# Kernel optimization log

Measured on AMD Instinct MI355X. Metric: run time of the kernel, lower is better.

The kernel has to match this reference:

```python
import jax, jax.numpy as jnp
import numpy as np

BETA = 0.3        # SmoothL1Loss beta
LAMBDA_PHY = 0.15 # physics loss weight


def smooth_l1(d, beta):
    ad = jnp.abs(d)
    return jnp.where(ad < beta, 0.5 * d * d / beta, ad - 0.5 * beta)


def setup_inputs() -> dict:
    key = jax.random.key(0)
    k1, k2, k3, k4 = jax.random.split(key, 4)
    B, Z = 16384, 2048
    preds = jax.random.normal(k1, (B, Z, 1), dtype=jnp.float32)
    targets = jax.random.normal(k2, (B, Z), dtype=jnp.float32)
    current_temps = jax.random.normal(k3, (B, Z), dtype=jnp.float32)
    adjacency = jax.random.randint(k4, (Z, Z), 0, 2).astype(jnp.int32)
    return {"preds": preds, "targets": targets,
            "current_temps": current_temps, "adjacency": adjacency}


def reference(preds, targets, current_temps, adjacency):
    p = preds[:, :, 0]                               # [B, Z]
    num_zones = p.shape[1]
    pred_loss = smooth_l1(p - targets, BETA).mean()
    pred_change = p - current_temps                  # [B, Z]

    # Vectorized neighbor mean: replaces the per-zone Python loop with one
    # dense masked-adjacency contraction.
    mask = (adjacency > 0).astype(p.dtype)           # [Z, Z]
    deg = mask.sum(axis=1)                           # [Z]
    has_nb = deg > 0
    safe_deg = jnp.where(has_nb, deg, 1.0)
    avg_neighbor = jnp.einsum('zn,bn->bz', mask, current_temps) / safe_deg  # [B, Z]

    temp_diff = current_temps - avg_neighbor         # [B, Z]
    violation = jax.nn.softplus(temp_diff * pred_change)
    per_zone = violation.mean(axis=0)                # mean over batch, [Z]
    physics_loss = jnp.where(has_nb, per_zone, 0.0).sum() / num_zones

    total_loss = pred_loss + LAMBDA_PHY * physics_loss
    return (total_loss, physics_loss)
```

## Files before the change

kernel.cpp:

```cpp
#include <hip/hip_runtime.h>
#include <hip/hip_bf16.h>
#include <cmath>

#define BETA 0.3f
#define LAMBDA_PHY 0.15f

#define BM 128
#define BN 128
#define BK 64
#define NT 256

typedef __bf16 bf16x8 __attribute__((ext_vector_type(8)));
typedef float f32x4 __attribute__((ext_vector_type(4)));

#define AS1 __attribute__((address_space(1)))
#define AS3 __attribute__((address_space(3)))

#define FENCE() asm volatile("" ::: "memory")
#define BARRIER() do { FENCE(); __builtin_amdgcn_s_barrier(); FENCE(); } while (0)
#define WAITV8() asm volatile("s_waitcnt vmcnt(8)" ::: "memory")
#define WAITV0() asm volatile("s_waitcnt vmcnt(0)" ::: "memory")

__device__ __forceinline__ unsigned short f2bf_rn(float f) {
    unsigned int u = __builtin_bit_cast(unsigned int, f);
    return (unsigned short)((u + 0x7FFFu + ((u >> 16) & 1u)) >> 16);
}

__device__ __forceinline__ float bf2f(unsigned short u) {
    return __builtin_bit_cast(float, (unsigned int)u << 16);
}

__device__ __forceinline__ float softplus_f(float x) {
    return fmaxf(x, 0.0f) + __logf(1.0f + __expf(-fabsf(x)));
}

__device__ __forceinline__ float smooth_l1_f(float d) {
    float ad = fabsf(d);
    return (ad < BETA) ? (0.5f / BETA) * d * d : (ad - 0.5f * BETA);
}

__global__ void k_prep(const int* __restrict__ adj, unsigned short* __restrict__ maskbf,
                       float* __restrict__ invdeg, float* __restrict__ hasnb, int Z) {
    int z = blockIdx.x;
    int t = threadIdx.x;
    const int* row = adj + (size_t)z * Z;
    unsigned short* mrow = maskbf + (size_t)z * Z;
    int cnt = 0;
    for (int n = t; n < Z; n += blockDim.x) {
        int a = (row[n] > 0);
        mrow[n] = a ? (unsigned short)0x3F80 : (unsigned short)0;
        cnt += a;
    }
    for (int o = 32; o; o >>= 1) cnt += __shfl_down(cnt, o);
    __shared__ int rs[4];
    int lane = t & 63, wave = t >> 6;
    if (lane == 0) rs[wave] = cnt;
    __syncthreads();
    if (t == 0) {
        int deg = rs[0] + rs[1] + rs[2] + rs[3];
        invdeg[z] = (deg > 0) ? 1.0f / (float)deg : 1.0f;
        hasnb[z]  = (deg > 0) ? 1.0f : 0.0f;
    }
}

__global__ void k_conv(const float* __restrict__ src, uint4* __restrict__ dst, long n8) {
    long i = (long)blockIdx.x * blockDim.x + threadIdx.x;
    long stride = (long)gridDim.x * blockDim.x;
    for (; i < n8; i += stride) {
        const float4* s = (const float4*)(src + i * 8);
        float4 a = s[0], b = s[1];
        uint4 o;
        o.x = (unsigned)f2bf_rn(a.x) | ((unsigned)f2bf_rn(a.y) << 16);
        o.y = (unsigned)f2bf_rn(a.z) | ((unsigned)f2bf_rn(a.w) << 16);
        o.z = (unsigned)f2bf_rn(b.x) | ((unsigned)f2bf_rn(b.y) << 16);
        o.w = (unsigned)f2bf_rn(b.z) | ((unsigned)f2bf_rn(b.w) << 16);
        dst[i] = o;
    }
}

__global__ __launch_bounds__(NT, 2) void k_gemm(
    const unsigned short* __restrict__ Abf,
    const unsigned short* __restrict__ Bbf,
    const float* __restrict__ preds,
    const float* __restrict__ targets,
    const float* __restrict__ invdeg,
    const float* __restrict__ hasnb,
    float* __restrict__ partials,
    int M, int N, int K)
{
    __shared__ unsigned short AsF[2 * BM * 64];
    __shared__ unsigned short BsF[2 * BN * 64];

    const int nwg = gridDim.x;
    const int ob = blockIdx.x;
    const int bid = (nwg % 8 == 0) ? ((ob % 8) * (nwg / 8) + ob / 8) : ob;
    const int ntiles = N / BN;
    const int mt = bid / ntiles;
    const int nt = bid % ntiles;
    const int row0 = mt * BM;
    const int col0 = nt * BN;
    const int t = threadIdx.x;
    const int lane = t & 63;
    const int wave = t >> 6;
    const int wm = wave >> 1;
    const int wn = wave & 1;
    const int fr = lane & 15;
    const int fq = lane >> 4;
    const int fr7 = fr & 7;

    const int tr = t >> 3;
    const int tc = t & 7;
    const int cs = tc ^ (tr & 7);

    const int colk0 = (fq ^ fr7) * 8;
    const int colk1 = ((4 + fq) ^ fr7) * 8;
    const int ofsA0 = (wm * 64 + fr) * 64 + colk0;
    const int ofsA1 = (wm * 64 + fr) * 64 + colk1;
    const int ofsB0 = (wn * 64 + fr) * 64 + colk0;
    const int ofsB1 = (wn * 64 + fr) * 64 + colk1;

    f32x4 acc[4][4];
#pragma unroll
    for (int m = 0; m < 4; ++m)
#pragma unroll
        for (int n = 0; n < 4; ++n)
            acc[m][n] = (f32x4){0.f, 0.f, 0.f, 0.f};

    const unsigned short* aSrc = Abf + (size_t)(row0 + tr) * K + cs * 8;
    const unsigned short* bSrc = Bbf + (size_t)(col0 + tr) * K + cs * 8;
    unsigned short* aDstC = &AsF[t * 8];
    unsigned short* bDstC = &BsF[t * 8];

#define STAGE(BUF) do {                                                                      \
    _Pragma("unroll")                                                                        \
    for (int r_ = 0; r_ < 4; ++r_)                                                           \
        __builtin_amdgcn_global_load_lds((const AS1 void*)(aSrc + (size_t)(r_ * 32) * K),    \
                                         (AS3 void*)(aDstC + (BUF) * 8192 + r_ * 2048), 16, 0, 0); \
    _Pragma("unroll")                                                                        \
    for (int r_ = 0; r_ < 4; ++r_)                                                           \
        __builtin_amdgcn_global_load_lds((const AS1 void*)(bSrc + (size_t)(r_ * 32) * K),    \
                                         (AS3 void*)(bDstC + (BUF) * 8192 + r_ * 2048), 16, 0, 0); \
    aSrc += BK; bSrc += BK;                                                                  \
} while (0)

#define MFMA_KK(BUF, OFSA, OFSB) do {                                                        \
    bf16x8 af_[4], bv_[4];                                                                   \
    _Pragma("unroll")                                                                        \
    for (int mi_ = 0; mi_ < 4; ++mi_)                                                        \
        af_[mi_] = *(const bf16x8*)(AsF + (BUF) * 8192 + (OFSA) + mi_ * 1024);               \
    _Pragma("unroll")                                                                        \
    for (int ni_ = 0; ni_ < 4; ++ni_)                                                        \
        bv_[ni_] = *(const bf16x8*)(BsF + (BUF) * 8192 + (OFSB) + ni_ * 1024);               \
    __builtin_amdgcn_s_setprio(1);                                                           \
    _Pragma("unroll")                                                                        \
    for (int mi_ = 0; mi_ < 4; ++mi_)                                                        \
    _Pragma("unroll")                                                                        \
    for (int ni_ = 0; ni_ < 4; ++ni_)                                                        \
        acc[mi_][ni_] = __builtin_amdgcn_mfma_f32_16x16x32_bf16(                             \
            af_[mi_], bv_[ni_], acc[mi_][ni_], 0, 0, 0);                                     \
    __builtin_amdgcn_s_setprio(0);                                                           \
} while (0)

    const int nk = K / BK;
    const int nk2 = nk >> 1;
    STAGE(0);

    for (int i = 0; i < nk2; ++i) {
        STAGE(1);
        WAITV8();
        BARRIER();
        MFMA_KK(0, ofsA0, ofsB0);
        MFMA_KK(0, ofsA1, ofsB1);
        BARRIER();
        if (i + 1 < nk2) {
            STAGE(0);
            WAITV8();
        } else {
            WAITV0();
        }
        BARRIER();
        MFMA_KK(1, ofsA0, ofsB0);
        MFMA_KK(1, ofsA1, ofsB1);
        BARRIER();
    }

#undef STAGE
#undef MFMA_KK

    float vsum = 0.f, ssum = 0.f;
#pragma unroll
    for (int n = 0; n < 4; ++n) {
        const int z = col0 + wn * 64 + n * 16 + fr;
        const float idg = invdeg[z];
        const float hnb = hasnb[z];
#pragma unroll
        for (int m = 0; m < 4; ++m) {
            const int rb = row0 + wm * 64 + m * 16 + fq * 4;
#pragma unroll
            for (int j = 0; j < 4; ++j) {
                const size_t idx = (size_t)(rb + j) * N + z;
                float avg = acc[m][n][j] * idg;
                float c = bf2f(Abf[idx]);
                float p = preds[idx];
                float tg = targets[idx];
                float x = (c - avg) * (p - c);
                vsum += softplus_f(x) * hnb;
                ssum += smooth_l1_f(p - tg);
            }
        }
    }
    for (int o = 32; o; o >>= 1) { vsum += __shfl_down(vsum, o); ssum += __shfl_down(ssum, o); }
    __shared__ float rv[4], rsm[4];
    if (lane == 0) { rv[wave] = vsum; rsm[wave] = ssum; }
    __syncthreads();
    if (t == 0) {
        partials[2 * (size_t)ob]     = rv[0] + rv[1] + rv[2] + rv[3];
        partials[2 * (size_t)ob + 1] = rsm[0] + rsm[1] + rsm[2] + rsm[3];
    }
}

__global__ void k_finalize(const float* __restrict__ partials, int nblk,
                           float* __restrict__ out, float invBZ) {
    __shared__ float sv[256], ss[256];
    int t = threadIdx.x;
    float v = 0.f, s = 0.f;
    for (int i = t; i < nblk; i += 256) { v += partials[2 * (size_t)i]; s += partials[2 * (size_t)i + 1]; }
    sv[t] = v; ss[t] = s;
    __syncthreads();
    for (int o = 128; o; o >>= 1) {
        if (t < o) { sv[t] += sv[t + o]; ss[t] += ss[t + o]; }
        __syncthreads();
    }
    if (t == 0) {
        float phys = sv[0] * invBZ;
        float pred = ss[0] * invBZ;
        out[0] = pred + LAMBDA_PHY * phys;
        out[1] = phys;
    }
}

__global__ void k_zero2(float* p) { if (threadIdx.x < 2) p[threadIdx.x] = 0.f; }

__global__ void k_fallback(const float* __restrict__ preds, const float* __restrict__ targets,
                           const float* __restrict__ ctemps, const int* __restrict__ adj,
                           float* __restrict__ acc2, int B, int Z) {
    extern __shared__ float crow[];
    int nzb = (Z + 255) / 256;
    int b = blockIdx.x / nzb;
    int zb = blockIdx.x % nzb;
    int t = threadIdx.x;
    const float* cr = ctemps + (size_t)b * Z;
    for (int n = t; n < Z; n += 256) crow[n] = cr[n];
    __syncthreads();
    int z = zb * 256 + t;
    float vsum = 0.f, ssum = 0.f;
    if (z < Z) {
        const int* arow = adj + (size_t)z * Z;
        float sum = 0.f; int deg = 0;
        for (int n = 0; n < Z; ++n) {
            if (arow[n] > 0) { sum += crow[n]; ++deg; }
        }
        float avg = (deg > 0) ? sum / (float)deg : 0.f;
        float c = crow[z];
        size_t idx = (size_t)b * Z + z;
        float p = preds[idx];
        float x = (c - avg) * (p - c);
        vsum = (deg > 0) ? softplus_f(x) : 0.f;
        ssum = smooth_l1_f(p - targets[idx]);
    }
    for (int o = 32; o; o >>= 1) { vsum += __shfl_down(vsum, o); ssum += __shfl_down(ssum, o); }
    __shared__ float rv[4], rs2[4];
    int lane = t & 63, wave = t >> 6;
    if (lane == 0) { rv[wave] = vsum; rs2[wave] = ssum; }
    __syncthreads();
    if (t == 0) {
        atomicAdd(&acc2[0], rv[0] + rv[1] + rv[2] + rv[3]);
        atomicAdd(&acc2[1], rs2[0] + rs2[1] + rs2[2] + rs2[3]);
    }
}

extern "C" void kernel_launch(void* const* d_in, const int* in_sizes, int n_in,
                              void* d_out, int out_size, void* d_ws, size_t ws_size,
                              hipStream_t stream) {
    const float* preds   = (const float*)d_in[0];
    const float* targets = (const float*)d_in[1];
    const float* ctemps  = (const float*)d_in[2];
    const int*   adj     = (const int*)d_in[3];
    float* out = (float*)d_out;

    long zz = in_sizes[3];
    int Z = (int)llround(sqrt((double)zz));
    int B = in_sizes[1] / Z;

    size_t off = 0;
    size_t maskOff = off; off += (size_t)Z * Z * 2;
    size_t cbfOff  = off; off += (size_t)B * Z * 2;
    size_t idgOff  = off; off += (size_t)Z * 4;
    size_t hnbOff  = off; off += (size_t)Z * 4;
    int nblk = (Z > 0 && B > 0 && (B % BM) == 0 && (Z % BN) == 0) ? (B / BM) * (Z / BN) : 0;
    size_t partOff = off; off += (size_t)(nblk > 0 ? nblk : 1) * 2 * 4;

    bool main_ok = (B % BM == 0) && (Z % BN == 0) && (Z % BK == 0) &&
                   (((Z / BK) % 2) == 0) && (ws_size >= off);

    float invBZ = (float)(1.0 / ((double)B * (double)Z));

    if (main_ok) {
        char* ws = (char*)d_ws;
        unsigned short* maskbf = (unsigned short*)(ws + maskOff);
        unsigned short* cbf    = (unsigned short*)(ws + cbfOff);
        float* idg      = (float*)(ws + idgOff);
        float* hnb      = (float*)(ws + hnbOff);
        float* partials = (float*)(ws + partOff);

        k_prep<<<Z, 256, 0, stream>>>(adj, maskbf, idg, hnb, Z);
        long n8 = (long)B * Z / 8;
        k_conv<<<2048, 256, 0, stream>>>(ctemps, (uint4*)cbf, n8);
        k_gemm<<<nblk, NT, 0, stream>>>(cbf, maskbf, preds, targets, idg, hnb, partials, B, Z, Z);
        k_finalize<<<1, 256, 0, stream>>>(partials, nblk, out, invBZ);
    } else {
        float* acc2 = (float*)d_ws;
        k_zero2<<<1, 64, 0, stream>>>(acc2);
        int nzb = (Z + 255) / 256;
        k_fallback<<<B * nzb, 256, (size_t)Z * 4, stream>>>(preds, targets, ctemps, adj, acc2, B, Z);
        k_finalize<<<1, 256, 0, stream>>>(acc2, 1, out, invBZ);
    }
}
```

Before: 230.9 us.

## Halve GEMM K-tile to raise occupancy and fuse prep with bf16 conversion

```diff
diff --git a/kernel.cpp b/kernel.cpp
--- a/kernel.cpp
+++ b/kernel.cpp
@@ -7,7 +7,7 @@
 
 #define BM 128
 #define BN 128
-#define BK 64
+#define BK 32
 #define NT 256
 
 typedef __bf16 bf16x8 __attribute__((ext_vector_type(8)));
@@ -18,7 +18,7 @@
 
 #define FENCE() asm volatile("" ::: "memory")
 #define BARRIER() do { FENCE(); __builtin_amdgcn_s_barrier(); FENCE(); } while (0)
-#define WAITV8() asm volatile("s_waitcnt vmcnt(8)" ::: "memory")
+#define WAITV4() asm volatile("s_waitcnt vmcnt(4)" ::: "memory")
 #define WAITV0() asm volatile("s_waitcnt vmcnt(0)" ::: "memory")
 
 __device__ __forceinline__ unsigned short f2bf_rn(float f) {
@@ -39,46 +39,48 @@
     return (ad < BETA) ? (0.5f / BETA) * d * d : (ad - 0.5f * BETA);
 }
 
-__global__ void k_prep(const int* __restrict__ adj, unsigned short* __restrict__ maskbf,
-                       float* __restrict__ invdeg, float* __restrict__ hasnb, int Z) {
-    int z = blockIdx.x;
+__global__ void k_prepconv(const int* __restrict__ adj, unsigned short* __restrict__ maskbf,
+                           float* __restrict__ invdeg, float* __restrict__ hasnb, int Z,
+                           const float* __restrict__ src, uint4* __restrict__ dst,
+                           long n8, int ncb) {
     int t = threadIdx.x;
-    const int* row = adj + (size_t)z * Z;
-    unsigned short* mrow = maskbf + (size_t)z * Z;
-    int cnt = 0;
-    for (int n = t; n < Z; n += blockDim.x) {
-        int a = (row[n] > 0);
-        mrow[n] = a ? (unsigned short)0x3F80 : (unsigned short)0;
-        cnt += a;
-    }
-    for (int o = 32; o; o >>= 1) cnt += __shfl_down(cnt, o);
-    __shared__ int rs[4];
-    int lane = t & 63, wave = t >> 6;
-    if (lane == 0) rs[wave] = cnt;
-    __syncthreads();
-    if (t == 0) {
-        int deg = rs[0] + rs[1] + rs[2] + rs[3];
-        invdeg[z] = (deg > 0) ? 1.0f / (float)deg : 1.0f;
-        hasnb[z]  = (deg > 0) ? 1.0f : 0.0f;
-    }
-}
-
-__global__ void k_conv(const float* __restrict__ src, uint4* __restrict__ dst, long n8) {
-    long i = (long)blockIdx.x * blockDim.x + threadIdx.x;
-    long stride = (long)gridDim.x * blockDim.x;
-    for (; i < n8; i += stride) {
-        const float4* s = (const float4*)(src + i * 8);
-        float4 a = s[0], b = s[1];
-        uint4 o;
-        o.x = (unsigned)f2bf_rn(a.x) | ((unsigned)f2bf_rn(a.y) << 16);
-        o.y = (unsigned)f2bf_rn(a.z) | ((unsigned)f2bf_rn(a.w) << 16);
-        o.z = (unsigned)f2bf_rn(b.x) | ((unsigned)f2bf_rn(b.y) << 16);
-        o.w = (unsigned)f2bf_rn(b.z) | ((unsigned)f2bf_rn(b.w) << 16);
-        dst[i] = o;
-    }
-}
-
-__global__ __launch_bounds__(NT, 2) void k_gemm(
+    if ((int)blockIdx.x < Z) {
+        int z = blockIdx.x;
+        const int* row = adj + (size_t)z * Z;
+        unsigned short* mrow = maskbf + (size_t)z * Z;
+        int cnt = 0;
+        for (int n = t; n < Z; n += blockDim.x) {
+            int a = (row[n] > 0);
+            mrow[n] = a ? (unsigned short)0x3F80 : (unsigned short)0;
+            cnt += a;
+        }
+        for (int o = 32; o; o >>= 1) cnt += __shfl_down(cnt, o);
+        __shared__ int rs[4];
+        int lane = t & 63, wave = t >> 6;
+        if (lane == 0) rs[wave] = cnt;
+        __syncthreads();
+        if (t == 0) {
+            int deg = rs[0] + rs[1] + rs[2] + rs[3];
+            invdeg[z] = (deg > 0) ? 1.0f / (float)deg : 1.0f;
+            hasnb[z]  = (deg > 0) ? 1.0f : 0.0f;
+        }
+    } else {
+        long i = (long)(blockIdx.x - Z) * blockDim.x + t;
+        long stride = (long)ncb * blockDim.x;
+        for (; i < n8; i += stride) {
+            const float4* s = (const float4*)(src + i * 8);
+            float4 a = s[0], b = s[1];
+            uint4 o;
+            o.x = (unsigned)f2bf_rn(a.x) | ((unsigned)f2bf_rn(a.y) << 16);
+            o.y = (unsigned)f2bf_rn(a.z) | ((unsigned)f2bf_rn(a.w) << 16);
+            o.z = (unsigned)f2bf_rn(b.x) | ((unsigned)f2bf_rn(b.y) << 16);
+            o.w = (unsigned)f2bf_rn(b.z) | ((unsigned)f2bf_rn(b.w) << 16);
+            dst[i] = o;
+        }
+    }
+}
+
+__global__ __launch_bounds__(NT, 4) void k_gemm(
     const unsigned short* __restrict__ Abf,
     const unsigned short* __restrict__ Bbf,
     const float* __restrict__ preds,
@@ -88,8 +90,8 @@
     float* __restrict__ partials,
     int M, int N, int K)
 {
-    __shared__ unsigned short AsF[2 * BM * 64];
-    __shared__ unsigned short BsF[2 * BN * 64];
+    __shared__ unsigned short AsF[2 * BM * BK];
+    __shared__ unsigned short BsF[2 * BN * BK];
 
     const int nwg = gridDim.x;
     const int ob = blockIdx.x;
@@ -106,18 +108,14 @@
     const int wn = wave & 1;
     const int fr = lane & 15;
     const int fq = lane >> 4;
-    const int fr7 = fr & 7;
-
-    const int tr = t >> 3;
-    const int tc = t & 7;
-    const int cs = tc ^ (tr & 7);
-
-    const int colk0 = (fq ^ fr7) * 8;
-    const int colk1 = ((4 + fq) ^ fr7) * 8;
-    const int ofsA0 = (wm * 64 + fr) * 64 + colk0;
-    const int ofsA1 = (wm * 64 + fr) * 64 + colk1;
-    const int ofsB0 = (wn * 64 + fr) * 64 + colk0;
-    const int ofsB1 = (wn * 64 + fr) * 64 + colk1;
+
+    const int tr = t >> 2;
+    const int tc = t & 3;
+    const int cs = tc ^ (tr & 3);
+
+    const int slot = (fq ^ (fr & 3)) * 8;
+    const int ofsA = (wm * 64 + fr) * BK + slot;
+    const int ofsB = (wn * 64 + fr) * BK + slot;
 
     f32x4 acc[4][4];
 #pragma unroll
@@ -132,25 +130,25 @@
     unsigned short* bDstC = &BsF[t * 8];
 
 #define STAGE(BUF) do {                                                                      \
-    _Pragma("unroll")                                                                        \
-    for (int r_ = 0; r_ < 4; ++r_)                                                           \
-        __builtin_amdgcn_global_load_lds((const AS1 void*)(aSrc + (size_t)(r_ * 32) * K),    \
-                                         (AS3 void*)(aDstC + (BUF) * 8192 + r_ * 2048), 16, 0, 0); \
-    _Pragma("unroll")                                                                        \
-    for (int r_ = 0; r_ < 4; ++r_)                                                           \
-        __builtin_amdgcn_global_load_lds((const AS1 void*)(bSrc + (size_t)(r_ * 32) * K),    \
-                                         (AS3 void*)(bDstC + (BUF) * 8192 + r_ * 2048), 16, 0, 0); \
+    __builtin_amdgcn_global_load_lds((const AS1 void*)(aSrc),                                \
+                                     (AS3 void*)(aDstC + (BUF) * 4096), 16, 0, 0);           \
+    __builtin_amdgcn_global_load_lds((const AS1 void*)(aSrc + (size_t)64 * K),               \
+                                     (AS3 void*)(aDstC + (BUF) * 4096 + 2048), 16, 0, 0);    \
+    __builtin_amdgcn_global_load_lds((const AS1 void*)(bSrc),                                \
+                                     (AS3 void*)(bDstC + (BUF) * 4096), 16, 0, 0);           \
+    __builtin_amdgcn_global_load_lds((const AS1 void*)(bSrc + (size_t)64 * K),               \
+                                     (AS3 void*)(bDstC + (BUF) * 4096 + 2048), 16, 0, 0);    \
     aSrc += BK; bSrc += BK;                                                                  \
 } while (0)
 
-#define MFMA_KK(BUF, OFSA, OFSB) do {                                                        \
+#define MFMA_TILE(BUF) do {                                                                  \
     bf16x8 af_[4], bv_[4];                                                                   \
     _Pragma("unroll")                                                                        \
     for (int mi_ = 0; mi_ < 4; ++mi_)                                                        \
-        af_[mi_] = *(const bf16x8*)(AsF + (BUF) * 8192 + (OFSA) + mi_ * 1024);               \
+        af_[mi_] = *(const bf16x8*)(AsF + (BUF) * 4096 + ofsA + mi_ * 512);                  \
     _Pragma("unroll")                                                                        \
     for (int ni_ = 0; ni_ < 4; ++ni_)                                                        \
-        bv_[ni_] = *(const bf16x8*)(BsF + (BUF) * 8192 + (OFSB) + ni_ * 1024);               \
+        bv_[ni_] = *(const bf16x8*)(BsF + (BUF) * 4096 + ofsB + ni_ * 512);                  \
     __builtin_amdgcn_s_setprio(1);                                                           \
     _Pragma("unroll")                                                                        \
     for (int mi_ = 0; mi_ < 4; ++mi_)                                                        \
@@ -167,25 +165,23 @@
 
     for (int i = 0; i < nk2; ++i) {
         STAGE(1);
-        WAITV8();
+        WAITV4();
         BARRIER();
-        MFMA_KK(0, ofsA0, ofsB0);
-        MFMA_KK(0, ofsA1, ofsB1);
+        MFMA_TILE(0);
         BARRIER();
         if (i + 1 < nk2) {
             STAGE(0);
-            WAITV8();
+            WAITV4();
         } else {
             WAITV0();
         }
         BARRIER();
-        MFMA_KK(1, ofsA0, ofsB0);
-        MFMA_KK(1, ofsA1, ofsB1);
+        MFMA_TILE(1);
         BARRIER();
     }
 
 #undef STAGE
-#undef MFMA_KK
+#undef MFMA_TILE
 
     float vsum = 0.f, ssum = 0.f;
 #pragma unroll
@@ -301,7 +297,7 @@
     size_t partOff = off; off += (size_t)(nblk > 0 ? nblk : 1) * 2 * 4;
 
     bool main_ok = (B % BM == 0) && (Z % BN == 0) && (Z % BK == 0) &&
-                   (((Z / BK) % 2) == 0) && (ws_size >= off);
+                   (((Z / BK) % 2) == 0) && ((B * Z) % 8 == 0) && (ws_size >= off);
 
     float invBZ = (float)(1.0 / ((double)B * (double)Z));
 
@@ -313,9 +309,10 @@
         float* hnb      = (float*)(ws + hnbOff);
         float* partials = (float*)(ws + partOff);
 
-        k_prep<<<Z, 256, 0, stream>>>(adj, maskbf, idg, hnb, Z);
         long n8 = (long)B * Z / 8;
-        k_conv<<<2048, 256, 0, stream>>>(ctemps, (uint4*)cbf, n8);
+        int ncb = 2048;
+        k_prepconv<<<Z + ncb, 256, 0, stream>>>(adj, maskbf, idg, hnb, Z,
+                                                ctemps, (uint4*)cbf, n8, ncb);
         k_gemm<<<nblk, NT, 0, stream>>>(cbf, maskbf, preds, targets, idg, hnb, partials, B, Z, Z);
         k_finalize<<<1, 256, 0, stream>>>(partials, nblk, out, invBZ);
     } else {
```

Measured after the change: 354.0 us. +53.3%, slower.
